# Performance work log

Hardware: AMD Instinct MI355X
Metric: run time of the kernel (lower is better)

## Reference

```python
import jax, jax.numpy as jnp
import numpy as np

N_HEADS = 12
EPS = 1e-6


def setup_inputs() -> dict:
    key = jax.random.key(0)
    ks = jax.random.split(key, 9)
    Bs, M, T, C = 2, 32, 1024, 768
    s = 1.0 / np.sqrt(C)
    return {
        "x": jax.random.normal(ks[0], (Bs, M, T, C), jnp.float32),
        "wq": jax.random.normal(ks[1], (C, C), jnp.float32) * s,
        "bq": jax.random.normal(ks[2], (C,), jnp.float32) * 0.02,
        "wk": jax.random.normal(ks[3], (C, C), jnp.float32) * s,
        "bk": jax.random.normal(ks[4], (C,), jnp.float32) * 0.02,
        "wv": jax.random.normal(ks[5], (C, C), jnp.float32) * s,
        "bv": jax.random.normal(ks[6], (C,), jnp.float32) * 0.02,
        "wp": jax.random.normal(ks[7], (C, C), jnp.float32) * s,
        "bp": jax.random.normal(ks[8], (C,), jnp.float32) * 0.02,
    }


def reference(x, wq, bq, wk, bk, wv, bv, wp, bp):
    Bs, M, T, C = x.shape
    N = N_HEADS
    D = C // N

    def heads(w, b):
        # [Bs,M,T,C] -> [Bs,M,N,T,D]
        y = x @ w.T + b
        return y.reshape(Bs, M, T, N, D).transpose(0, 1, 3, 2, 4)

    q = jax.nn.elu(heads(wq, bq)) + 1.0
    k = jax.nn.elu(heads(wk, bk)) + 1.0
    v = heads(wv, bv)

    # KtV: [Bs,M,N,D,D]
    KtV = jnp.einsum('bmntd,bmnte->bmnde', k, v)
    ksum = k.sum(axis=3)                                   # [Bs,M,N,D]
    z = 1.0 / (jnp.einsum('bmntd,bmnd->bmnt', q, ksum) + EPS)  # [Bs,M,N,T]
    # Faithful to source: Z expanded over D is constant per row, so
    # V[t,e] = z_t * sum_d KtV[d,e]
    s = KtV.sum(axis=-2)                                   # [Bs,M,N,D]
    V = z[..., None] * s[:, :, :, None, :]                 # [Bs,M,N,T,D]
    V = V.transpose(0, 1, 3, 2, 4).reshape(Bs, M, T, N * D)
    out = V @ wp.T + bp
    return out
```

## Files before the change

kernel.cpp:

```cpp
#include <hip/hip_runtime.h>
#include <hip/hip_bf16.h>


typedef float f32x4 __attribute__((ext_vector_type(4)));
typedef short s16x4 __attribute__((ext_vector_type(4)));
typedef short s16x8 __attribute__((ext_vector_type(8)));

__device__ __forceinline__ short f2bf(float f) {
    unsigned u = __builtin_bit_cast(unsigned, f);
    u = (u + 0x7fffu + ((u >> 16) & 1u)) >> 16;
    return (short)u;
}

#define WS_KSUM 0u
#define WS_XK   49152u
#define WS_KR   638976u
#define WS_Z    1425408u
#define WS_U    2211840u
#define WS_F32_FLOATS 2801664u
#define XB_ELEMS 50331648ull
#define WB_ELEMS 589824ull
#define WS_NEED_BYTES (WS_F32_FLOATS * 4ull + (XB_ELEMS + 2ull * WB_ELEMS) * 2ull)

#define GLL16(g, l)                                                             \
    __builtin_amdgcn_global_load_lds(                                           \
        (const __attribute__((address_space(1))) unsigned int*)(g),             \
        (__attribute__((address_space(3))) unsigned int*)(l), 16, 0, 0)

__global__ __launch_bounds__(256)
void conv_kernel(const float* __restrict__ in, short* __restrict__ out, int n8)
{
    int i = blockIdx.x * 256 + threadIdx.x;
    const int stride = gridDim.x * 256;
    for (; i < n8; i += stride) {
        f32x4 a = ((const f32x4*)in)[2 * i];
        f32x4 b = ((const f32x4*)in)[2 * i + 1];
        s16x8 o;
        o[0] = f2bf(a[0]); o[1] = f2bf(a[1]); o[2] = f2bf(a[2]); o[3] = f2bf(a[3]);
        o[4] = f2bf(b[0]); o[5] = f2bf(b[1]); o[6] = f2bf(b[2]); o[7] = f2bf(b[3]);
        ((s16x8*)out)[i] = o;
    }
}

template<int MODE>
__global__ __launch_bounds__(256, 2)
void gemm_bf16_kernel(const short* __restrict__ xb, const short* __restrict__ wb,
                      const float* __restrict__ bias, float* __restrict__ ksum,
                      float* __restrict__ aux)
{
    __shared__ alignas(16) short As[128][32];
    __shared__ alignas(16) short Bsh[128][32];

    const int bid = blockIdx.x;
    const int swz = (bid & 7) * 384 + (bid >> 3);
    const int ct = swz % 6;
    const int rt = swz / 6;
    const int bm = rt >> 3;
    const int t0loc = (rt & 7) << 7;
    const int tid = threadIdx.x;
    const int lane = tid & 63;
    const int w = tid >> 6;
    const int wm = w >> 1, wn = w & 1;

    const int r0 = w * 32 + (lane >> 2);
    const int r1 = r0 + 16;
    const int ga = lane & 3;
    const int c0 = (ga ^ ((r0 >> 1) & 3)) << 3;
    const int c1 = (ga ^ ((r1 >> 1) & 3)) << 3;
    const short* pA0 = xb + (long)(rt * 128 + r0) * 768 + c0;
    const short* pA1 = xb + (long)(rt * 128 + r1) * 768 + c1;
    const short* pB0 = wb + (long)(ct * 128 + r0) * 768 + c0;
    const short* pB1 = wb + (long)(ct * 128 + r1) * 768 + c1;
    short* ldsA0 = &As[w * 32][0];
    short* ldsA1 = &As[w * 32 + 16][0];
    short* ldsB0 = &Bsh[w * 32][0];
    short* ldsB1 = &Bsh[w * 32 + 16][0];

    const int fr = lane & 15, g = lane >> 4;
    int offAlo[4], offAhi[4], offBlo[4], offBhi[4];
#pragma unroll
    for (int m = 0; m < 4; ++m) {
        const int rA = wm * 64 + m * 16 + fr;
        const int sa = (rA >> 1) & 3;
        offAlo[m] = rA * 64 + ((((g >> 1) + 0) ^ sa) << 4) + ((g & 1) << 3);
        offAhi[m] = rA * 64 + ((((g >> 1) + 2) ^ sa) << 4) + ((g & 1) << 3);
        const int rB = wn * 64 + m * 16 + fr;
        const int sb = (rB >> 1) & 3;
        offBlo[m] = rB * 64 + ((((g >> 1) + 0) ^ sb) << 4) + ((g & 1) << 3);
        offBhi[m] = rB * 64 + ((((g >> 1) + 2) ^ sb) << 4) + ((g & 1) << 3);
    }
    const char* ldsAb = (const char*)&As[0][0];
    const char* ldsBb = (const char*)&Bsh[0][0];

    f32x4 acc[4][4];
#pragma unroll
    for (int m = 0; m < 4; ++m)
#pragma unroll
        for (int n = 0; n < 4; ++n)
            acc[m][n] = f32x4{0.f, 0.f, 0.f, 0.f};

    for (int k0 = 0; k0 < 768; k0 += 32) {
        GLL16(pA0 + k0, ldsA0);
        GLL16(pA1 + k0, ldsA1);
        GLL16(pB0 + k0, ldsB0);
        GLL16(pB1 + k0, ldsB1);
        __syncthreads();
        s16x8 af[4], bfr[4];
#pragma unroll
        for (int m = 0; m < 4; ++m) {
            s16x4 lo = *(const s16x4*)(ldsAb + offAlo[m]);
            s16x4 hi = *(const s16x4*)(ldsAb + offAhi[m]);
            af[m] = __builtin_shufflevector(lo, hi, 0, 1, 2, 3, 4, 5, 6, 7);
        }
#pragma unroll
        for (int n = 0; n < 4; ++n) {
            s16x4 lo = *(const s16x4*)(ldsBb + offBlo[n]);
            s16x4 hi = *(const s16x4*)(ldsBb + offBhi[n]);
            bfr[n] = __builtin_shufflevector(lo, hi, 0, 1, 2, 3, 4, 5, 6, 7);
        }
#pragma unroll
        for (int m = 0; m < 4; ++m)
#pragma unroll
            for (int n = 0; n < 4; ++n)
                acc[m][n] = __builtin_amdgcn_mfma_f32_16x16x32_bf16(af[m], bfr[n], acc[m][n], 0, 0, 0);
        __syncthreads();
    }

    const int head = ct * 2 + wn;

    if (MODE == 0) {
        float rowsum[4][4] = {};
#pragma unroll
        for (int n = 0; n < 4; ++n) {
            const int colg = ct * 128 + wn * 64 + n * 16 + fr;
            const float bkv = bias[colg];
            float colsum = 0.f;
#pragma unroll
            for (int m = 0; m < 4; ++m)
#pragma unroll
                for (int j = 0; j < 4; ++j) {
                    float v = acc[m][n][j] + bkv;
                    float kv = v > 0.f ? v + 1.f : __expf(v);
                    colsum += kv;
                    rowsum[m][j] += kv;
                }
            colsum += __shfl_xor(colsum, 16);
            colsum += __shfl_xor(colsum, 32);
            if (lane < 16) atomicAdd(&ksum[(long)bm * 768 + colg], colsum);
        }
#pragma unroll
        for (int m = 0; m < 4; ++m)
#pragma unroll
            for (int j = 0; j < 4; ++j) {
                float r = rowsum[m][j];
                r += __shfl_xor(r, 1); r += __shfl_xor(r, 2);
                r += __shfl_xor(r, 4); r += __shfl_xor(r, 8);
                if (fr == 0) {
                    const int t = t0loc + wm * 64 + m * 16 + (lane >> 4) * 4 + j;
                    aux[((long)bm * 1024 + t) * 12 + head] = r;
                }
            }
    } else {
        float zdot[4][4] = {};
#pragma unroll
        for (int n = 0; n < 4; ++n) {
            const int colg = ct * 128 + wn * 64 + n * 16 + fr;
            const float bqv = bias[colg];
            const float ksv = ksum[(long)bm * 768 + colg];
#pragma unroll
            for (int m = 0; m < 4; ++m)
#pragma unroll
                for (int j = 0; j < 4; ++j) {
                    float v = acc[m][n][j] + bqv;
                    float qv = v > 0.f ? v + 1.f : __expf(v);
                    zdot[m][j] += qv * ksv;
                }
        }
#pragma unroll
        for (int m = 0; m < 4; ++m)
#pragma unroll
            for (int j = 0; j < 4; ++j) {
                float r = zdot[m][j];
                r += __shfl_xor(r, 1); r += __shfl_xor(r, 2);
                r += __shfl_xor(r, 4); r += __shfl_xor(r, 8);
                if (fr == 0) {
                    const int t = t0loc + wm * 64 + m * 16 + (lane >> 4) * 4 + j;
                    aux[((long)bm * 1024 + t) * 12 + head] = 1.f / (r + 1e-6f);
                }
            }
    }
}

template<int MODE>
__global__ __launch_bounds__(256, 2)
void gemm_act_kernel(const float* __restrict__ x, const float* __restrict__ w,
                     const float* __restrict__ bias, float* __restrict__ ksum,
                     float* __restrict__ aux)
{
    __shared__ alignas(16) short As[128][40];
    __shared__ alignas(16) short Bs[128][40];

    const int ct = blockIdx.x % 6;
    const int rt = blockIdx.x / 6;
    const int bm = rt >> 3;
    const int t0 = (rt & 7) << 7;
    const int tid = threadIdx.x;
    const int lane = tid & 63;
    const int wid = tid >> 6;
    const int wm = wid >> 1;
    const int wn = wid & 1;

    f32x4 acc[4][4];
#pragma unroll
    for (int m = 0; m < 4; ++m)
#pragma unroll
        for (int n = 0; n < 4; ++n)
            acc[m][n] = f32x4{0.f, 0.f, 0.f, 0.f};

    const int srow = tid >> 3;
    const int kq   = (tid & 7) << 2;
    const int p    = ((kq >> 2) & 3) * 8 + (kq >> 4) * 4;

    const float* xp = x + ((long)bm * 1024 + t0) * 768 + kq;
    const float* wp_ = w + (long)(ct * 128) * 768 + kq;

    for (int k0 = 0; k0 < 768; k0 += 32) {
#pragma unroll
        for (int r = 0; r < 4; ++r) {
            const int row = srow + r * 32;
            f32x4 a4 = *(const f32x4*)(xp + (long)row * 768 + k0);
            f32x4 b4 = *(const f32x4*)(wp_ + (long)row * 768 + k0);
            s16x4 av, bv;
            av[0] = f2bf(a4[0]); av[1] = f2bf(a4[1]); av[2] = f2bf(a4[2]); av[3] = f2bf(a4[3]);
            bv[0] = f2bf(b4[0]); bv[1] = f2bf(b4[1]); bv[2] = f2bf(b4[2]); bv[3] = f2bf(b4[3]);
            *(s16x4*)&As[row][p] = av;
            *(s16x4*)&Bs[row][p] = bv;
        }
        __syncthreads();
        const int g8 = (lane >> 4) << 3;
        const int fr = lane & 15;
        s16x8 af[4], bf8[4];
#pragma unroll
        for (int m = 0; m < 4; ++m)
            af[m] = *(const s16x8*)&As[wm * 64 + m * 16 + fr][g8];
#pragma unroll
        for (int n = 0; n < 4; ++n)
            bf8[n] = *(const s16x8*)&Bs[wn * 64 + n * 16 + fr][g8];
#pragma unroll
        for (int m = 0; m < 4; ++m)
#pragma unroll
            for (int n = 0; n < 4; ++n)
                acc[m][n] = __builtin_amdgcn_mfma_f32_16x16x32_bf16(af[m], bf8[n], acc[m][n], 0, 0, 0);
        __syncthreads();
    }

    const int fr = lane & 15;
    const int head = ct * 2 + wn;

    if (MODE == 0) {
        float rowsum[4][4] = {};
#pragma unroll
        for (int n = 0; n < 4; ++n) {
            const int colg = ct * 128 + wn * 64 + n * 16 + fr;
            const float bkv = bias[colg];
            float colsum = 0.f;
#pragma unroll
            for (int m = 0; m < 4; ++m)
#pragma unroll
                for (int j = 0; j < 4; ++j) {
                    float v = acc[m][n][j] + bkv;
                    float kv = v > 0.f ? v + 1.f : __expf(v);
                    colsum += kv;
                    rowsum[m][j] += kv;
                }
            colsum += __shfl_xor(colsum, 16);
            colsum += __shfl_xor(colsum, 32);
            if (lane < 16) atomicAdd(&ksum[(long)bm * 768 + colg], colsum);
        }
#pragma unroll
        for (int m = 0; m < 4; ++m)
#pragma unroll
            for (int j = 0; j < 4; ++j) {
                float r = rowsum[m][j];
                r += __shfl_xor(r, 1); r += __shfl_xor(r, 2);
                r += __shfl_xor(r, 4); r += __shfl_xor(r, 8);
                if (fr == 0) {
                    const int t = t0 + wm * 64 + m * 16 + (lane >> 4) * 4 + j;
                    aux[((long)bm * 1024 + t) * 12 + head] = r;
                }
            }
    } else {
        float zdot[4][4] = {};
#pragma unroll
        for (int n = 0; n < 4; ++n) {
            const int colg = ct * 128 + wn * 64 + n * 16 + fr;
            const float bqv = bias[colg];
            const float ksv = ksum[(long)bm * 768 + colg];
#pragma unroll
            for (int m = 0; m < 4; ++m)
#pragma unroll
                for (int j = 0; j < 4; ++j) {
                    float v = acc[m][n][j] + bqv;
                    float qv = v > 0.f ? v + 1.f : __expf(v);
                    zdot[m][j] += qv * ksv;
                }
        }
#pragma unroll
        for (int m = 0; m < 4; ++m)
#pragma unroll
            for (int j = 0; j < 4; ++j) {
                float r = zdot[m][j];
                r += __shfl_xor(r, 1); r += __shfl_xor(r, 2);
                r += __shfl_xor(r, 4); r += __shfl_xor(r, 8);
                if (fr == 0) {
                    const int t = t0 + wm * 64 + m * 16 + (lane >> 4) * 4 + j;
                    aux[((long)bm * 1024 + t) * 12 + head] = 1.f / (r + 1e-6f);
                }
            }
    }
}

__global__ __launch_bounds__(256)
void xk_kernel(const float* __restrict__ x, const float* __restrict__ kr,
               float* __restrict__ xk)
{
    __shared__ float krs[128][12];
    const int bm = blockIdx.x >> 3;
    const int t0 = (blockIdx.x & 7) << 7;
    const int tid = threadIdx.x;

    float* krsf = &krs[0][0];
    for (int i = tid; i < 1536; i += 256)
        krsf[i] = kr[((long)bm * 1024 + t0) * 12 + i];
    __syncthreads();

    float acc[3][12] = {};
    const float* xp = x + ((long)bm * 1024 + t0) * 768;
#pragma unroll 2
    for (int t = 0; t < 128; ++t) {
        const float x0 = xp[(long)t * 768 + tid];
        const float x1 = xp[(long)t * 768 + 256 + tid];
        const float x2 = xp[(long)t * 768 + 512 + tid];
#pragma unroll
        for (int n = 0; n < 12; ++n) {
            const float kv = krs[t][n];
            acc[0][n] += kv * x0;
            acc[1][n] += kv * x1;
            acc[2][n] += kv * x2;
        }
    }
#pragma unroll
    for (int i = 0; i < 3; ++i)
#pragma unroll
        for (int n = 0; n < 12; ++n)
            atomicAdd(&xk[((long)bm * 12 + n) * 768 + i * 256 + tid], acc[i][n]);
}

__global__ __launch_bounds__(256)
void su_kernel(const float* __restrict__ xk, const float* __restrict__ ksum,
               const float* __restrict__ wv, const float* __restrict__ bv,
               const float* __restrict__ wp, float* __restrict__ u)
{
    __shared__ float xks[768];
    __shared__ float red[4][64];
    __shared__ float sl[64];
    __shared__ float krtot_s;
    const int bm = blockIdx.x / 12;
    const int n = blockIdx.x % 12;
    const int tid = threadIdx.x;

    for (int i = tid; i < 768; i += 256)
        xks[i] = xk[((long)bm * 12 + n) * 768 + i];
    if (tid < 64) {
        float v = ksum[(long)bm * 768 + n * 64 + tid];
        for (int m = 1; m < 64; m <<= 1) v += __shfl_xor(v, m);
        if (tid == 0) krtot_s = v;
    }
    __syncthreads();

    const int e = tid & 63, pp = tid >> 6;
    const float* wvr = wv + (long)(n * 64 + e) * 768;
    float sp = 0.f;
    for (int c = pp * 192; c < pp * 192 + 192; ++c) sp += xks[c] * wvr[c];
    red[pp][e] = sp;
    __syncthreads();
    if (tid < 64) {
        sl[tid] = red[0][tid] + red[1][tid] + red[2][tid] + red[3][tid]
                + krtot_s * bv[n * 64 + tid];
    }
    __syncthreads();

#pragma unroll
    for (int i = 0; i < 3; ++i) {
        const int c = i * 256 + tid;
        const float* wpr = wp + (long)c * 768 + n * 64;
        float uv = 0.f;
#pragma unroll
        for (int ee = 0; ee < 64; ++ee) uv += sl[ee] * wpr[ee];
        u[((long)bm * 12 + n) * 768 + c] = uv;
    }
}

__global__ __launch_bounds__(256)
void out_kernel(const float* __restrict__ z, const float* __restrict__ u,
                const float* __restrict__ bp, float* __restrict__ out)
{
    __shared__ float us[12][768];
    __shared__ float zs[16][12];
    const int bm = blockIdx.x >> 6;
    const int t0 = (blockIdx.x & 63) << 4;
    const int tid = threadIdx.x;

    float* usf = &us[0][0];
    for (int i = tid; i < 9216; i += 256)
        usf[i] = u[(long)bm * 9216 + i];
    float* zsf = &zs[0][0];
    for (int i = tid; i < 192; i += 256)
        zsf[i] = z[((long)bm * 1024 + t0) * 12 + i];
    __syncthreads();

    const float b0 = bp[tid], b1 = bp[256 + tid], b2 = bp[512 + tid];
    for (int r = 0; r < 16; ++r) {
        float zr[12];
#pragma unroll
        for (int nn = 0; nn < 12; ++nn) zr[nn] = zs[r][nn];
        float v0 = b0, v1 = b1, v2 = b2;
#pragma unroll
        for (int nn = 0; nn < 12; ++nn) {
            v0 += zr[nn] * us[nn][tid];
            v1 += zr[nn] * us[nn][256 + tid];
            v2 += zr[nn] * us[nn][512 + tid];
        }
        const long o = ((long)bm * 1024 + t0 + r) * 768;
        out[o + tid] = v0;
        out[o + 256 + tid] = v1;
        out[o + 512 + tid] = v2;
    }
}

extern "C" void kernel_launch(void* const* d_in, const int* in_sizes, int n_in,
                              void* d_out, int out_size, void* d_ws, size_t ws_size,
                              hipStream_t stream)
{
    const float* x  = (const float*)d_in[0];
    const float* wq = (const float*)d_in[1];
    const float* bq = (const float*)d_in[2];
    const float* wk = (const float*)d_in[3];
    const float* bk = (const float*)d_in[4];
    const float* wv = (const float*)d_in[5];
    const float* bv = (const float*)d_in[6];
    const float* wp = (const float*)d_in[7];
    const float* bp = (const float*)d_in[8];
    float* out = (float*)d_out;
    float* ws = (float*)d_ws;

    float* ksum = ws + WS_KSUM;
    float* xk   = ws + WS_XK;
    float* kr   = ws + WS_KR;
    float* z    = ws + WS_Z;
    float* u    = ws + WS_U;

    hipMemsetAsync(ksum, 0, (size_t)(49152 + 589824) * sizeof(float), stream);

    if (ws_size >= WS_NEED_BYTES) {
        short* xbb = (short*)(ws + WS_F32_FLOATS);
        short* wkb = xbb + XB_ELEMS;
        short* wqb = wkb + WB_ELEMS;

        conv_kernel<<<2048, 256, 0, stream>>>(x, xbb, 6291456);
        conv_kernel<<<288, 256, 0, stream>>>(wk, wkb, 73728);
        conv_kernel<<<288, 256, 0, stream>>>(wq, wqb, 73728);

        gemm_bf16_kernel<0><<<3072, 256, 0, stream>>>(xbb, wkb, bk, ksum, kr);
        xk_kernel<<<512, 256, 0, stream>>>(x, kr, xk);
        su_kernel<<<768, 256, 0, stream>>>(xk, ksum, wv, bv, wp, u);
        gemm_bf16_kernel<1><<<3072, 256, 0, stream>>>(xbb, wqb, bq, ksum, z);
        out_kernel<<<4096, 256, 0, stream>>>(z, u, bp, out);
    } else {
        gemm_act_kernel<0><<<3072, 256, 0, stream>>>(x, wk, bk, ksum, kr);
        xk_kernel<<<512, 256, 0, stream>>>(x, kr, xk);
        su_kernel<<<768, 256, 0, stream>>>(xk, ksum, wv, bv, wp, u);
        gemm_act_kernel<1><<<3072, 256, 0, stream>>>(x, wq, bq, ksum, z);
        out_kernel<<<4096, 256, 0, stream>>>(z, u, bp, out);
    }
}
```

Measured before the change: 737.7 us.

## Pre-permute bf16 layout for single 16B LDS reads, split su kernel, retune occupancy

The fp32-to-bf16 conversion now permutes each 32-element K chunk, so every MFMA fragment becomes a single contiguous 16-byte LDS read instead of two 8-byte reads plus a shuffle. The GEMM launch bound rises to 4 waves per SIMD. xk_kernel processes 256 rows per block, halving the number of atomic adds. The su kernel is split into an s-computation kernel with vectorized wv loads and a separate u kernel that reads wp rows coalesced and reduces with shuffles. The extra kernel launch and workspace buffer add some overhead, and the higher occupancy target may force register spills.

Result: no change. 748.1 us (+1.4%).

```diff
diff --git a/kernel.cpp b/kernel.cpp
--- a/kernel.cpp
+++ b/kernel.cpp
@@ -17,9 +17,12 @@
 #define WS_KR   638976u
 #define WS_Z    1425408u
 #define WS_U    2211840u
-#define WS_F32_FLOATS 2801664u
+#define WS_S    2801664u
+#define WS_F32_FLOATS 2850816u
 #define XB_ELEMS 50331648ull
 #define WB_ELEMS 589824ull
+#define XB_GRAN 6291456
+#define WB_GRAN 73728
 #define WS_NEED_BYTES (WS_F32_FLOATS * 4ull + (XB_ELEMS + 2ull * WB_ELEMS) * 2ull)
 
 #define GLL16(g, l)                                                             \
@@ -28,13 +31,18 @@
         (__attribute__((address_space(3))) unsigned int*)(l), 16, 0, 0)
 
 __global__ __launch_bounds__(256)
-void conv_kernel(const float* __restrict__ in, short* __restrict__ out, int n8)
+void convp_kernel(const float* __restrict__ in, short* __restrict__ out, int ngran)
 {
     int i = blockIdx.x * 256 + threadIdx.x;
     const int stride = gridDim.x * 256;
-    for (; i < n8; i += stride) {
-        f32x4 a = ((const f32x4*)in)[2 * i];
-        f32x4 b = ((const f32x4*)in)[2 * i + 1];
+    for (; i < ngran; i += stride) {
+        const int row = i / 96;
+        const int gr  = i - row * 96;
+        const int c   = gr >> 2;
+        const int g   = gr & 3;
+        const float* p = in + (long)row * 768 + c * 32 + g * 4;
+        f32x4 a = *(const f32x4*)p;
+        f32x4 b = *(const f32x4*)(p + 16);
         s16x8 o;
         o[0] = f2bf(a[0]); o[1] = f2bf(a[1]); o[2] = f2bf(a[2]); o[3] = f2bf(a[3]);
         o[4] = f2bf(b[0]); o[5] = f2bf(b[1]); o[6] = f2bf(b[2]); o[7] = f2bf(b[3]);
@@ -43,7 +51,7 @@
 }
 
 template<int MODE>
-__global__ __launch_bounds__(256, 2)
+__global__ __launch_bounds__(256, 4)
 void gemm_bf16_kernel(const short* __restrict__ xb, const short* __restrict__ wb,
                       const float* __restrict__ bias, float* __restrict__ ksum,
                       float* __restrict__ aux)
@@ -77,17 +85,13 @@
     short* ldsB1 = &Bsh[w * 32 + 16][0];
 
     const int fr = lane & 15, g = lane >> 4;
-    int offAlo[4], offAhi[4], offBlo[4], offBhi[4];
+    int offA[4], offB[4];
 #pragma unroll
     for (int m = 0; m < 4; ++m) {
         const int rA = wm * 64 + m * 16 + fr;
-        const int sa = (rA >> 1) & 3;
-        offAlo[m] = rA * 64 + ((((g >> 1) + 0) ^ sa) << 4) + ((g & 1) << 3);
-        offAhi[m] = rA * 64 + ((((g >> 1) + 2) ^ sa) << 4) + ((g & 1) << 3);
+        offA[m] = rA * 64 + ((g ^ ((rA >> 1) & 3)) << 4);
         const int rB = wn * 64 + m * 16 + fr;
-        const int sb = (rB >> 1) & 3;
-        offBlo[m] = rB * 64 + ((((g >> 1) + 0) ^ sb) << 4) + ((g & 1) << 3);
-        offBhi[m] = rB * 64 + ((((g >> 1) + 2) ^ sb) << 4) + ((g & 1) << 3);
+        offB[m] = rB * 64 + ((g ^ ((rB >> 1) & 3)) << 4);
     }
     const char* ldsAb = (const char*)&As[0][0];
     const char* ldsBb = (const char*)&Bsh[0][0];
@@ -107,17 +111,11 @@
         __syncthreads();
         s16x8 af[4], bfr[4];
 #pragma unroll
-        for (int m = 0; m < 4; ++m) {
-            s16x4 lo = *(const s16x4*)(ldsAb + offAlo[m]);
-            s16x4 hi = *(const s16x4*)(ldsAb + offAhi[m]);
-            af[m] = __builtin_shufflevector(lo, hi, 0, 1, 2, 3, 4, 5, 6, 7);
-        }
-#pragma unroll
-        for (int n = 0; n < 4; ++n) {
-            s16x4 lo = *(const s16x4*)(ldsBb + offBlo[n]);
-            s16x4 hi = *(const s16x4*)(ldsBb + offBhi[n]);
-            bfr[n] = __builtin_shufflevector(lo, hi, 0, 1, 2, 3, 4, 5, 6, 7);
-        }
+        for (int m = 0; m < 4; ++m)
+            af[m] = *(const s16x8*)(ldsAb + offA[m]);
+#pragma unroll
+        for (int n = 0; n < 4; ++n)
+            bfr[n] = *(const s16x8*)(ldsBb + offB[n]);
 #pragma unroll
         for (int m = 0; m < 4; ++m)
 #pragma unroll
@@ -324,20 +322,19 @@
 void xk_kernel(const float* __restrict__ x, const float* __restrict__ kr,
                float* __restrict__ xk)
 {
-    __shared__ float krs[128][12];
-    const int bm = blockIdx.x >> 3;
-    const int t0 = (blockIdx.x & 7) << 7;
+    __shared__ float krs[256][12];
+    const int bm = blockIdx.x >> 2;
+    const int t0 = (blockIdx.x & 3) << 8;
     const int tid = threadIdx.x;
 
     float* krsf = &krs[0][0];
-    for (int i = tid; i < 1536; i += 256)
+    for (int i = tid; i < 3072; i += 256)
         krsf[i] = kr[((long)bm * 1024 + t0) * 12 + i];
     __syncthreads();
 
     float acc[3][12] = {};
     const float* xp = x + ((long)bm * 1024 + t0) * 768;
-#pragma unroll 2
-    for (int t = 0; t < 128; ++t) {
+    for (int t = 0; t < 256; ++t) {
         const float x0 = xp[(long)t * 768 + tid];
         const float x1 = xp[(long)t * 768 + 256 + tid];
         const float x2 = xp[(long)t * 768 + 512 + tid];
@@ -357,13 +354,12 @@
 }
 
 __global__ __launch_bounds__(256)
-void su_kernel(const float* __restrict__ xk, const float* __restrict__ ksum,
-               const float* __restrict__ wv, const float* __restrict__ bv,
-               const float* __restrict__ wp, float* __restrict__ u)
+void su_s_kernel(const float* __restrict__ xk, const float* __restrict__ ksum,
+                 const float* __restrict__ wv, const float* __restrict__ bv,
+                 float* __restrict__ s_out)
 {
     __shared__ float xks[768];
     __shared__ float red[4][64];
-    __shared__ float sl[64];
     __shared__ float krtot_s;
     const int bm = blockIdx.x / 12;
     const int n = blockIdx.x % 12;
@@ -381,23 +377,59 @@
     const int e = tid & 63, pp = tid >> 6;
     const float* wvr = wv + (long)(n * 64 + e) * 768;
     float sp = 0.f;
-    for (int c = pp * 192; c < pp * 192 + 192; ++c) sp += xks[c] * wvr[c];
+    for (int c = pp * 192; c < pp * 192 + 192; c += 4) {
+        f32x4 wv4 = *(const f32x4*)(wvr + c);
+        sp += xks[c] * wv4[0] + xks[c + 1] * wv4[1]
+            + xks[c + 2] * wv4[2] + xks[c + 3] * wv4[3];
+    }
     red[pp][e] = sp;
     __syncthreads();
     if (tid < 64) {
-        sl[tid] = red[0][tid] + red[1][tid] + red[2][tid] + red[3][tid]
-                + krtot_s * bv[n * 64 + tid];
-    }
+        s_out[(long)bm * 768 + n * 64 + tid] =
+            red[0][tid] + red[1][tid] + red[2][tid] + red[3][tid]
+            + krtot_s * bv[n * 64 + tid];
+    }
+}
+
+__global__ __launch_bounds__(256)
+void su_u_kernel(const float* __restrict__ s, const float* __restrict__ wp,
+                 float* __restrict__ u)
+{
+    __shared__ float sl[768];
+    const int bm = blockIdx.x >> 2;
+    const int quarter = blockIdx.x & 3;
+    const int tid = threadIdx.x;
+    const int l = tid & 63, w = tid >> 6;
+
+    for (int i = tid; i < 768; i += 256)
+        sl[i] = s[(long)bm * 768 + i];
     __syncthreads();
 
-#pragma unroll
-    for (int i = 0; i < 3; ++i) {
-        const int c = i * 256 + tid;
-        const float* wpr = wp + (long)c * 768 + n * 64;
-        float uv = 0.f;
-#pragma unroll
-        for (int ee = 0; ee < 64; ++ee) uv += sl[ee] * wpr[ee];
-        u[((long)bm * 12 + n) * 768 + c] = uv;
+    f32x4 sv0 = *(const f32x4*)&sl[4 * l];
+    f32x4 sv1 = *(const f32x4*)&sl[256 + 4 * l];
+    f32x4 sv2 = *(const f32x4*)&sl[512 + 4 * l];
+    const int h = l >> 4;
+
+    for (int r = 0; r < 48; ++r) {
+        const int c = quarter * 192 + w * 48 + r;
+        const float* row = wp + (long)c * 768;
+        f32x4 a = *(const f32x4*)(row + 4 * l);
+        f32x4 b = *(const f32x4*)(row + 256 + 4 * l);
+        f32x4 d = *(const f32x4*)(row + 512 + 4 * l);
+        float p0 = a[0] * sv0[0] + a[1] * sv0[1] + a[2] * sv0[2] + a[3] * sv0[3];
+        float p1 = b[0] * sv1[0] + b[1] * sv1[1] + b[2] * sv1[2] + b[3] * sv1[3];
+        float p2 = d[0] * sv2[0] + d[1] * sv2[1] + d[2] * sv2[2] + d[3] * sv2[3];
+        p0 += __shfl_xor(p0, 1); p0 += __shfl_xor(p0, 2);
+        p0 += __shfl_xor(p0, 4); p0 += __shfl_xor(p0, 8);
+        p1 += __shfl_xor(p1, 1); p1 += __shfl_xor(p1, 2);
+        p1 += __shfl_xor(p1, 4); p1 += __shfl_xor(p1, 8);
+        p2 += __shfl_xor(p2, 1); p2 += __shfl_xor(p2, 2);
+        p2 += __shfl_xor(p2, 4); p2 += __shfl_xor(p2, 8);
+        if ((l & 15) == 0) {
+            u[((long)bm * 12 + h) * 768 + c] = p0;
+            u[((long)bm * 12 + h + 4) * 768 + c] = p1;
+            u[((long)bm * 12 + h + 8) * 768 + c] = p2;
+        }
     }
 }
 
@@ -459,6 +491,7 @@
     float* kr   = ws + WS_KR;
     float* z    = ws + WS_Z;
     float* u    = ws + WS_U;
+    float* s    = ws + WS_S;
 
     hipMemsetAsync(ksum, 0, (size_t)(49152 + 589824) * sizeof(float), stream);
 
@@ -467,19 +500,21 @@
         short* wkb = xbb + XB_ELEMS;
         short* wqb = wkb + WB_ELEMS;
 
-        conv_kernel<<<2048, 256, 0, stream>>>(x, xbb, 6291456);
-        conv_kernel<<<288, 256, 0, stream>>>(wk, wkb, 73728);
-        conv_kernel<<<288, 256, 0, stream>>>(wq, wqb, 73728);
+        convp_kernel<<<2048, 256, 0, stream>>>(x, xbb, XB_GRAN);
+        convp_kernel<<<288, 256, 0, stream>>>(wk, wkb, WB_GRAN);
+        convp_kernel<<<288, 256, 0, stream>>>(wq, wqb, WB_GRAN);
 
         gemm_bf16_kernel<0><<<3072, 256, 0, stream>>>(xbb, wkb, bk, ksum, kr);
-        xk_kernel<<<512, 256, 0, stream>>>(x, kr, xk);
-        su_kernel<<<768, 256, 0, stream>>>(xk, ksum, wv, bv, wp, u);
+        xk_kernel<<<256, 256, 0, stream>>>(x, kr, xk);
+        su_s_kernel<<<768, 256, 0, stream>>>(xk, ksum, wv, bv, s);
+        su_u_kernel<<<256, 256, 0, stream>>>(s, wp, u);
         gemm_bf16_kernel<1><<<3072, 256, 0, stream>>>(xbb, wqb, bq, ksum, z);
         out_kernel<<<4096, 256, 0, stream>>>(z, u, bp, out);
     } else {
         gemm_act_kernel<0><<<3072, 256, 0, stream>>>(x, wk, bk, ksum, kr);
-        xk_kernel<<<512, 256, 0, stream>>>(x, kr, xk);
-        su_kernel<<<768, 256, 0, stream>>>(xk, ksum, wv, bv, wp, u);
+        xk_kernel<<<256, 256, 0, stream>>>(x, kr, xk);
+        su_s_kernel<<<768, 256, 0, stream>>>(xk, ksum, wv, bv, s);
+        su_u_kernel<<<256, 256, 0, stream>>>(s, wp, u);
         gemm_act_kernel<1><<<3072, 256, 0, stream>>>(x, wq, bq, ksum, z);
         out_kernel<<<4096, 256, 0, stream>>>(z, u, bp, out);
     }
```
